# Kernel optimization log

Measured on AMD Instinct MI355X. Metric: run time of the kernel, lower is better.

## Reference

```python
import jax, jax.numpy as jnp
import numpy as np

MARGIN = 0.0
GAP = 0.4
N, D, C = 8192, 128, 10


def setup_inputs() -> dict:
    key = jax.random.key(0)
    k1, k2, k3 = jax.random.split(key, 3)
    inputs = jax.random.normal(k1, (N, D), dtype=jnp.float32)
    pred = jax.random.normal(k2, (N, C), dtype=jnp.float32)
    targets = jax.random.randint(k3, (N,), 0, C, dtype=jnp.int64)
    return {"inputs": inputs, "pred": pred, "targets": targets}


def reference(inputs, pred, targets):
    n = inputs.shape[0]
    # pairwise euclidean distances: ||xi||^2 + ||xj||^2 - 2 xi.xj, clamped + sqrt
    sq = jnp.sum(inputs * inputs, axis=1)                      # [n]
    dist = sq[:, None] + sq[None, :] - 2.0 * (inputs @ inputs.T)
    dist = jnp.sqrt(jnp.clip(dist, 1e-12))                     # [n, n]
    same = targets[:, None] == targets[None, :]                # [n, n] bool

    # confusion detection (original runs under no_grad)
    p = jax.nn.softmax(jax.lax.stop_gradient(pred), axis=1)
    val, top2 = jax.lax.top_k(p, 2)                            # [n,2]
    confuse = (val[:, 0] - val[:, 1] <= GAP) | (top2[:, 0] != targets)  # [n]

    # hard mining per row: hardest positive (max over same-class), hardest negative (min over diff-class)
    dist_ap = jnp.max(jnp.where(same, dist, -jnp.inf), axis=1)  # [n]
    dist_an = jnp.min(jnp.where(same, jnp.inf, dist), axis=1)   # [n]

    # MarginRankingLoss(margin=MARGIN) with y=1: mean(relu(-(an - ap) + margin)) over confused rows
    per_row = jnp.maximum(dist_ap - dist_an + MARGIN, 0.0)
    cnt = jnp.sum(confuse.astype(jnp.float32))
    loss = jnp.sum(jnp.where(confuse, per_row, 0.0)) / jnp.maximum(cnt, 1.0)
    return jnp.where(cnt > 0, loss, 0.0)
```

## Files before the change

kernel.cpp:

```cpp
#include <hip/hip_runtime.h>

#define NROWS 8192
#define DIMX  128
#define KB    192
#define KSEG  12
#define PTB   24576
#define NKS   3
#define NCLS  10
#define GAPV  0.4f
#define DEBIAS 504.03125f
#define SCL   (-0.0078125f)
#define RGR   256
#define NRG   (NROWS / RGR)
#define CHUNK 512
#define NCHUNK (NROWS / CHUNK)
#define SLAB  64
#define NSLAB (CHUNK / SLAB)

typedef __attribute__((ext_vector_type(4))) int i32x4;

#define GLOAD_LDS16(g, l)                                              \
  __builtin_amdgcn_global_load_lds(                                    \
      (const __attribute__((address_space(1))) void*)(g),              \
      (__attribute__((address_space(3))) void*)(l), 16, 0, 0)

__device__ __forceinline__ unsigned fenc(float f) {
  unsigned u = __float_as_uint(f);
  return (u & 0x80000000u) ? ~u : (u | 0x80000000u);
}
__device__ __forceinline__ float fdec(unsigned u) {
  return (u & 0x80000000u) ? __uint_as_float(u & 0x7fffffffu) : __uint_as_float(~u);
}
__device__ __forceinline__ int q8(float v) {
  int q = (int)rintf(16.f * v);
  return q > 127 ? 127 : (q < -127 ? -127 : q);
}

__global__ __launch_bounds__(256) void prep_k(const float* __restrict__ x,
                                              const int* __restrict__ tgt,
                                              const float* __restrict__ pred,
                                              char* __restrict__ xa,
                                              char* __restrict__ xbm,
                                              float* __restrict__ sq,
                                              unsigned* __restrict__ emax,
                                              unsigned* __restrict__ emin,
                                              int* __restrict__ conf,
                                              unsigned* __restrict__ ctrs) {
  if (blockIdx.x == 0 && threadIdx.x < NRG + 3) ctrs[threadIdx.x] = 0u;

  const int wave = threadIdx.x >> 6;
  const int lane = threadIdx.x & 63;
  const int row  = blockIdx.x * 4 + wave;
  const float2 f2 = ((const float2*)(x + (size_t)row * DIMX))[lane];
  float s = f2.x * f2.x + f2.y * f2.y;
  #pragma unroll
  for (int m = 1; m < 64; m <<= 1) s += __shfl_xor(s, m, 64);

  char* basea = xa  + (size_t)(row >> 7) * PTB + (size_t)(row & 127) * 16;
  char* baseb = xbm + (size_t)(row >> 7) * PTB + (size_t)(row & 127) * 16;
  {
    const int q0 = q8(f2.x), q1 = q8(f2.y);
    const unsigned short u = (unsigned short)((q0 & 0xFF) | ((q1 & 0xFF) << 8));
    const size_t off = (size_t)(lane >> 3) * 2048 + (lane & 7) * 2;
    *(unsigned short*)(basea + off) = u;
    *(unsigned short*)(baseb + off) = u;
  }
  const int cls = tgt[row];
  if (lane < 32) {
    const int j = 2 * lane;
    const int c = j >> 2;
    const bool hit = (c < NCLS) && (c == cls);
    const unsigned short ua = hit ? (unsigned short)0x7F7F : 0;
    const unsigned short ub = hit ? (unsigned short)0x8181 : 0;
    const size_t off = (size_t)(8 + (j >> 4)) * 2048 + (j & 15);
    *(unsigned short*)(basea + off) = ua;
    *(unsigned short*)(baseb + off) = ub;
  }

  if (lane == 0) {
    sq[row]   = s;
    emax[row] = fenc(-INFINITY);
    emin[row] = fenc(INFINITY);
    const float* pp = pred + (size_t)row * NCLS;
    float v[NCLS];
    #pragma unroll
    for (int c = 0; c < NCLS; ++c) v[c] = pp[c];
    float m1 = v[0]; int i1 = 0;
    #pragma unroll
    for (int c = 1; c < NCLS; ++c)
      if (v[c] > m1) { m1 = v[c]; i1 = c; }
    float m2 = -INFINITY, sum = 0.f;
    #pragma unroll
    for (int c = 0; c < NCLS; ++c) {
      sum += __expf(v[c] - m1);
      if (c != i1) m2 = fmaxf(m2, v[c]);
    }
    const float d01 = (1.f - __expf(m2 - m1)) / sum;
    conf[row] = (d01 <= GAPV) || (i1 != cls);
  }
}

__global__ __launch_bounds__(256, 2) void gram_k(const char* __restrict__ xa,
                                                 const char* __restrict__ xbm,
                                                 const float* __restrict__ sq,
                                                 const int* __restrict__ conf,
                                                 unsigned* __restrict__ emax,
                                                 unsigned* __restrict__ emin,
                                                 unsigned* __restrict__ ctrs,
                                                 float* __restrict__ out) {
  __shared__ char  ldsb[2][KSEG * 1024];
  __shared__ float sqb[2][SLAB];
  __shared__ float red[2][4];
  __shared__ int   flag;
  const int tid  = threadIdx.x;
  const int wave = tid >> 6;
  const int lane = tid & 63;
  const int quad = lane >> 4;
  const int m16  = lane & 15;
  const int bx = blockIdx.x, by = blockIdx.y;
  const int i0 = bx * RGR + wave * 64;

  unsigned* rg_done = ctrs;
  unsigned* g_done  = ctrs + NRG;
  float*    Ssum    = (float*)(ctrs + NRG + 1);
  float*    Csum    = (float*)(ctrs + NRG + 2);

  i32x4 A[4][NKS];
  #pragma unroll
  for (int rt = 0; rt < 4; ++rt) {
    const int rbase = wave * 64 + rt * 16;
    const char* pa = xa + (size_t)(bx * 2 + (rbase >> 7)) * PTB
                        + (size_t)((rbase & 127) + m16) * 16;
    #pragma unroll
    for (int ks = 0; ks < NKS; ++ks)
      A[rt][ks] = *(const i32x4*)(pa + (size_t)(ks * 4 + quad) * 2048);
  }
  #pragma unroll
  for (int rt = 0; rt < 4; ++rt)
    #pragma unroll
    for (int ks = 0; ks < NKS; ++ks)
      asm("" : "+v"(A[rt][ks]));

  float gmin[4][4], gmax[4][4];
  #pragma unroll
  for (int r = 0; r < 4; ++r)
    #pragma unroll
    for (int q = 0; q < 4; ++q) { gmin[r][q] = INFINITY; gmax[r][q] = -INFINITY; }

  {
    const char* srcb = xbm + (size_t)(by * 4) * PTB;
    #pragma unroll
    for (int u = 0; u < 3; ++u) {
      const int kseg = wave * 3 + u;
      GLOAD_LDS16(srcb + (size_t)kseg * 2048 + lane * 16, &ldsb[0][kseg * 1024 + lane * 16]);
    }
    if (wave == 3 && lane < 16)
      GLOAD_LDS16((const char*)(sq + by * CHUNK) + lane * 16, (char*)&sqb[0][0] + lane * 16);
  }

  for (int s = 0; s < NSLAB; ++s) {
    __syncthreads();
    if (s + 1 < NSLAB) {
      const char* srcb = xbm + (size_t)(by * 4 + ((s + 1) >> 1)) * PTB + ((s + 1) & 1) * 1024;
      char* dstb = &ldsb[(s + 1) & 1][0];
      #pragma unroll
      for (int u = 0; u < 3; ++u) {
        const int kseg = wave * 3 + u;
        GLOAD_LDS16(srcb + (size_t)kseg * 2048 + lane * 16, dstb + kseg * 1024 + lane * 16);
      }
      if (wave == 3 && lane < 16)
        GLOAD_LDS16((const char*)(sq + by * CHUNK + (s + 1) * SLAB) + lane * 16,
                    (char*)&sqb[(s + 1) & 1][0] + lane * 16);
    }
    const char* buf = &ldsb[s & 1][0];
    #pragma unroll
    for (int jt = 0; jt < 4; ++jt) {
      i32x4 B[NKS];
      #pragma unroll
      for (int ks = 0; ks < NKS; ++ks)
        B[ks] = *(const i32x4*)(buf + (ks * 4 + quad) * 1024 + (jt * 16 + m16) * 16);
      const float sqj = sqb[s & 1][jt * 16 + m16];

      i32x4 acc[4];
      #pragma unroll
      for (int r = 0; r < 4; ++r) acc[r] = (i32x4){0, 0, 0, 0};
      #pragma unroll
      for (int ks = 0; ks < NKS; ++ks)
        #pragma unroll
        for (int r = 0; r < 4; ++r)
          acc[r] = __builtin_amdgcn_mfma_i32_16x16x64_i8(A[r][ks], B[ks], acc[r], 0, 0, 0);

      #pragma unroll
      for (int r = 0; r < 4; ++r)
        #pragma unroll
        for (int q = 0; q < 4; ++q) {
          const float cand = fmaf((float)acc[r][q], SCL, sqj);
          gmin[r][q] = fminf(gmin[r][q], cand);
          gmax[r][q] = fmaxf(gmax[r][q], cand);
        }
    }
  }

  #pragma unroll
  for (int m = 1; m <= 8; m <<= 1)
    #pragma unroll
    for (int r = 0; r < 4; ++r)
      #pragma unroll
      for (int q = 0; q < 4; ++q) {
        gmin[r][q] = fminf(gmin[r][q], __shfl_xor(gmin[r][q], m, 64));
        gmax[r][q] = fmaxf(gmax[r][q], __shfl_xor(gmax[r][q], m, 64));
      }

  if (m16 == 0) {
    #pragma unroll
    for (int r = 0; r < 4; ++r)
      #pragma unroll
      for (int q = 0; q < 4; ++q) {
        const int row = i0 + r * 16 + quad * 4 + q;
        atomicMax(&emax[row], fenc(gmax[r][q]));
        atomicMin(&emin[row], fenc(gmin[r][q]));
      }
  }

  __syncthreads();
  if (tid == 0) {
    __threadfence();
    flag = (atomicAdd(&rg_done[bx], 1u) == NCHUNK - 1u);
  }
  __syncthreads();
  if (!flag) return;
  __threadfence();

  const int row = bx * RGR + tid;
  float ps = 0.f, pc = 0.f;
  if (conf[row]) {
    const float hi = fdec(atomicMax(&emax[row], 0u));
    const float lo = fdec(atomicMin(&emin[row], 0xFFFFFFFFu));
    const float ap = sqrtf(fmaxf(sq[row] + hi - DEBIAS, 1e-12f));
    const float an = sqrtf(fmaxf(sq[row] + lo, 1e-12f));
    ps = fmaxf(ap - an, 0.f);
    pc = 1.f;
  }
  #pragma unroll
  for (int m = 1; m < 64; m <<= 1) {
    ps += __shfl_xor(ps, m, 64);
    pc += __shfl_xor(pc, m, 64);
  }
  if (lane == 0) { red[0][wave] = ps; red[1][wave] = pc; }
  __syncthreads();
  if (tid == 0) {
    float S = red[0][0] + red[0][1] + red[0][2] + red[0][3];
    float C = red[1][0] + red[1][1] + red[1][2] + red[1][3];
    atomicAdd(Ssum, S);
    atomicAdd(Csum, C);
    __threadfence();
    if (atomicAdd(g_done, 1u) == NRG - 1u) {
      const float St = atomicAdd(Ssum, 0.f);
      const float Ct = atomicAdd(Csum, 0.f);
      out[0] = (Ct > 0.f) ? (St / fmaxf(Ct, 1.f)) : 0.f;
    }
  }
}

extern "C" void kernel_launch(void* const* d_in, const int* in_sizes, int n_in,
                              void* d_out, int out_size, void* d_ws, size_t ws_size,
                              hipStream_t stream) {
  const float* x    = (const float*)d_in[0];
  const float* pred = (const float*)d_in[1];
  const int*   tgt  = (const int*)d_in[2];
  float* out = (float*)d_out;

  char* w = (char*)d_ws;
  const size_t arr_bytes = (size_t)NROWS * KB;
  char*     xa   = w;
  char*     xbm  = w + arr_bytes;
  float*    sq   = (float*)(w + 2 * arr_bytes);
  unsigned* emax = (unsigned*)(w + 2 * arr_bytes + (size_t)NROWS * 4);
  unsigned* emin = (unsigned*)(w + 2 * arr_bytes + (size_t)NROWS * 8);
  int*      conf = (int*)(w + 2 * arr_bytes + (size_t)NROWS * 12);
  unsigned* ctrs = (unsigned*)(w + 2 * arr_bytes + (size_t)NROWS * 16);

  hipLaunchKernelGGL(prep_k, dim3(NROWS / 4), dim3(256), 0, stream,
                     x, tgt, pred, xa, xbm, sq, emax, emin, conf, ctrs);
  hipLaunchKernelGGL(gram_k, dim3(NRG, NCHUNK), dim3(256), 0, stream,
                     xa, xbm, sq, conf, emax, emin, ctrs, out);
}
```

Measured before the change: 88.84 us.

## Replace per-row atomic min/max and last-block detection with staged partials and reduce kernel

The gram kernel no longer does per-row atomicMax/atomicMin on encoded floats or counts finished blocks per row group. Each block now writes its partial row max/min as float4 stores into a staging buffer indexed by (row group, chunk). A new third kernel reduces the 16 chunk partials per row and computes the loss. This removes the atomic contention and the threadfence/flag tail. The cost is an extra kernel launch and about 2 MB of staging traffic.

```diff
diff --git a/kernel.cpp b/kernel.cpp
--- a/kernel.cpp
+++ b/kernel.cpp
@@ -24,13 +24,6 @@
       (const __attribute__((address_space(1))) void*)(g),              \
       (__attribute__((address_space(3))) void*)(l), 16, 0, 0)
 
-__device__ __forceinline__ unsigned fenc(float f) {
-  unsigned u = __float_as_uint(f);
-  return (u & 0x80000000u) ? ~u : (u | 0x80000000u);
-}
-__device__ __forceinline__ float fdec(unsigned u) {
-  return (u & 0x80000000u) ? __uint_as_float(u & 0x7fffffffu) : __uint_as_float(~u);
-}
 __device__ __forceinline__ int q8(float v) {
   int q = (int)rintf(16.f * v);
   return q > 127 ? 127 : (q < -127 ? -127 : q);
@@ -42,11 +35,9 @@
                                               char* __restrict__ xa,
                                               char* __restrict__ xbm,
                                               float* __restrict__ sq,
-                                              unsigned* __restrict__ emax,
-                                              unsigned* __restrict__ emin,
                                               int* __restrict__ conf,
                                               unsigned* __restrict__ ctrs) {
-  if (blockIdx.x == 0 && threadIdx.x < NRG + 3) ctrs[threadIdx.x] = 0u;
+  if (blockIdx.x == 0 && threadIdx.x < 3) ctrs[threadIdx.x] = 0u;
 
   const int wave = threadIdx.x >> 6;
   const int lane = threadIdx.x & 63;
@@ -78,9 +69,7 @@
   }
 
   if (lane == 0) {
-    sq[row]   = s;
-    emax[row] = fenc(-INFINITY);
-    emin[row] = fenc(INFINITY);
+    sq[row] = s;
     const float* pp = pred + (size_t)row * NCLS;
     float v[NCLS];
     #pragma unroll
@@ -103,27 +92,16 @@
 __global__ __launch_bounds__(256, 2) void gram_k(const char* __restrict__ xa,
                                                  const char* __restrict__ xbm,
                                                  const float* __restrict__ sq,
-                                                 const int* __restrict__ conf,
-                                                 unsigned* __restrict__ emax,
-                                                 unsigned* __restrict__ emin,
-                                                 unsigned* __restrict__ ctrs,
-                                                 float* __restrict__ out) {
+                                                 float* __restrict__ smax,
+                                                 float* __restrict__ smin) {
   __shared__ char  ldsb[2][KSEG * 1024];
   __shared__ float sqb[2][SLAB];
-  __shared__ float red[2][4];
-  __shared__ int   flag;
   const int tid  = threadIdx.x;
   const int wave = tid >> 6;
   const int lane = tid & 63;
   const int quad = lane >> 4;
   const int m16  = lane & 15;
   const int bx = blockIdx.x, by = blockIdx.y;
-  const int i0 = bx * RGR + wave * 64;
-
-  unsigned* rg_done = ctrs;
-  unsigned* g_done  = ctrs + NRG;
-  float*    Ssum    = (float*)(ctrs + NRG + 1);
-  float*    Csum    = (float*)(ctrs + NRG + 2);
 
   i32x4 A[4][NKS];
   #pragma unroll
@@ -212,30 +190,39 @@
       }
 
   if (m16 == 0) {
-    #pragma unroll
-    for (int r = 0; r < 4; ++r)
-      #pragma unroll
-      for (int q = 0; q < 4; ++q) {
-        const int row = i0 + r * 16 + quad * 4 + q;
-        atomicMax(&emax[row], fenc(gmax[r][q]));
-        atomicMin(&emin[row], fenc(gmin[r][q]));
-      }
-  }
-
-  __syncthreads();
-  if (tid == 0) {
-    __threadfence();
-    flag = (atomicAdd(&rg_done[bx], 1u) == NCHUNK - 1u);
-  }
-  __syncthreads();
-  if (!flag) return;
-  __threadfence();
-
+    const size_t sidx = (size_t)(bx * NCHUNK + by) * RGR;
+    #pragma unroll
+    for (int r = 0; r < 4; ++r) {
+      const int lrow = wave * 64 + r * 16 + quad * 4;
+      *(float4*)&smax[sidx + lrow] = make_float4(gmax[r][0], gmax[r][1], gmax[r][2], gmax[r][3]);
+      *(float4*)&smin[sidx + lrow] = make_float4(gmin[r][0], gmin[r][1], gmin[r][2], gmin[r][3]);
+    }
+  }
+}
+
+__global__ __launch_bounds__(256) void reduce_k(const float* __restrict__ smax,
+                                                const float* __restrict__ smin,
+                                                const float* __restrict__ sq,
+                                                const int* __restrict__ conf,
+                                                unsigned* __restrict__ ctrs,
+                                                float* __restrict__ out) {
+  __shared__ float red[2][4];
+  const int tid = threadIdx.x, bx = blockIdx.x;
+  const int wave = tid >> 6, lane = tid & 63;
   const int row = bx * RGR + tid;
+
+  unsigned* g_done = ctrs;
+  float*    Ssum   = (float*)(ctrs + 1);
+  float*    Csum   = (float*)(ctrs + 2);
+
+  float hi = -INFINITY, lo = INFINITY;
+  #pragma unroll
+  for (int c = 0; c < NCHUNK; ++c) {
+    hi = fmaxf(hi, smax[(size_t)(bx * NCHUNK + c) * RGR + tid]);
+    lo = fminf(lo, smin[(size_t)(bx * NCHUNK + c) * RGR + tid]);
+  }
   float ps = 0.f, pc = 0.f;
   if (conf[row]) {
-    const float hi = fdec(atomicMax(&emax[row], 0u));
-    const float lo = fdec(atomicMin(&emin[row], 0xFFFFFFFFu));
     const float ap = sqrtf(fmaxf(sq[row] + hi - DEBIAS, 1e-12f));
     const float an = sqrtf(fmaxf(sq[row] + lo, 1e-12f));
     ps = fmaxf(ap - an, 0.f);
@@ -249,10 +236,8 @@
   if (lane == 0) { red[0][wave] = ps; red[1][wave] = pc; }
   __syncthreads();
   if (tid == 0) {
-    float S = red[0][0] + red[0][1] + red[0][2] + red[0][3];
-    float C = red[1][0] + red[1][1] + red[1][2] + red[1][3];
-    atomicAdd(Ssum, S);
-    atomicAdd(Csum, C);
+    atomicAdd(Ssum, red[0][0] + red[0][1] + red[0][2] + red[0][3]);
+    atomicAdd(Csum, red[1][0] + red[1][1] + red[1][2] + red[1][3]);
     __threadfence();
     if (atomicAdd(g_done, 1u) == NRG - 1u) {
       const float St = atomicAdd(Ssum, 0.f);
@@ -272,16 +257,19 @@
 
   char* w = (char*)d_ws;
   const size_t arr_bytes = (size_t)NROWS * KB;
+  const size_t stg_bytes = (size_t)NRG * NCHUNK * RGR * 4;
   char*     xa   = w;
   char*     xbm  = w + arr_bytes;
   float*    sq   = (float*)(w + 2 * arr_bytes);
-  unsigned* emax = (unsigned*)(w + 2 * arr_bytes + (size_t)NROWS * 4);
-  unsigned* emin = (unsigned*)(w + 2 * arr_bytes + (size_t)NROWS * 8);
-  int*      conf = (int*)(w + 2 * arr_bytes + (size_t)NROWS * 12);
-  unsigned* ctrs = (unsigned*)(w + 2 * arr_bytes + (size_t)NROWS * 16);
+  int*      conf = (int*)(w + 2 * arr_bytes + (size_t)NROWS * 4);
+  float*    smax = (float*)(w + 2 * arr_bytes + (size_t)NROWS * 8);
+  float*    smin = (float*)(w + 2 * arr_bytes + (size_t)NROWS * 8 + stg_bytes);
+  unsigned* ctrs = (unsigned*)(w + 2 * arr_bytes + (size_t)NROWS * 8 + 2 * stg_bytes);
 
   hipLaunchKernelGGL(prep_k, dim3(NROWS / 4), dim3(256), 0, stream,
-                     x, tgt, pred, xa, xbm, sq, emax, emin, conf, ctrs);
+                     x, tgt, pred, xa, xbm, sq, conf, ctrs);
   hipLaunchKernelGGL(gram_k, dim3(NRG, NCHUNK), dim3(256), 0, stream,
-                     xa, xbm, sq, conf, emax, emin, ctrs, out);
-}
+                     xa, xbm, sq, smax, smin);
+  hipLaunchKernelGGL(reduce_k, dim3(NRG), dim3(256), 0, stream,
+                     smax, smin, sq, conf, ctrs, out);
+}
```

Result: faster. 84.61 us (-4.8%).
